# Kernel optimization log

Hardware: AMD Instinct MI355X
Metric: run time of the kernel (lower is better)

## Reference

```python
import jax, jax.numpy as jnp
import numpy as np

B, S, D = 16, 1024, 512
H, DH = 8, 64  # heads, dim_head


def setup_inputs() -> dict:
    key = jax.random.key(0)
    ks = jax.random.split(key, 7)
    x = jax.random.normal(ks[0], (B, S, D), dtype=jnp.float32)
    # variable sequence lengths in [1, S]
    seq_lens = jnp.maximum(jax.random.randint(ks[1], (B,), 0, S + 1), 1).astype(jnp.int32)
    w_std = 0.02
    Wq = jax.random.normal(ks[2], (D, D), dtype=jnp.float32) * w_std
    Wk = jax.random.normal(ks[3], (D, D), dtype=jnp.float32) * w_std
    Wv = jax.random.normal(ks[4], (D, D), dtype=jnp.float32) * w_std
    Wo = jax.random.normal(ks[5], (D, D), dtype=jnp.float32) * w_std
    bo = jnp.zeros((D,), dtype=jnp.float32)
    return {"x": x, "seq_lens": seq_lens, "Wq": Wq, "Wk": Wk, "Wv": Wv, "Wo": Wo, "bo": bo}


def reference(x, seq_lens, Wq, Wk, Wv, Wo, bo):
    # x: [B, S, D] padded ragged batch; seq_lens: [B] valid token counts.
    # Equivalent to the per-batch SDPA loop over jagged sequences: attention
    # is computed only among the valid tokens of each sequence.
    scale = DH ** -0.5
    q = (x @ Wq).reshape(B, S, H, DH)
    k = (x @ Wk).reshape(B, S, H, DH)
    v = (x @ Wv).reshape(B, S, H, DH)
    scores = jnp.einsum('bqhd,bkhd->bhqk', q, k) * scale  # [B,H,S,S]
    valid = jnp.arange(S)[None, :] < seq_lens[:, None]     # [B,S] token mask
    neg_inf = jnp.finfo(scores.dtype).min
    scores = jnp.where(valid[:, None, None, :], scores, neg_inf)
    attn = jax.nn.softmax(scores, axis=-1)
    out = jnp.einsum('bhqk,bkhd->bqhd', attn, v).reshape(B, S, D)
    out = out @ Wo + bo  # to_out Linear (dropout=0 / eval)
    return out * valid[:, :, None]  # zero padded query positions
```

## Files before the change

kernel.cpp:

```cpp
#include <hip/hip_runtime.h>
#include <hip/hip_bf16.h>

typedef __bf16 bf16_t;
typedef __attribute__((ext_vector_type(4))) __bf16 bf16x4;
typedef __attribute__((ext_vector_type(8))) __bf16 bf16x8;
typedef __attribute__((ext_vector_type(4))) float f32x4;

#define MFMA16(a, b, c) __builtin_amdgcn_mfma_f32_16x16x32_bf16((a), (b), (c), 0, 0, 0)

#define BB 16
#define SS 1024
#define DD 512
#define HH 8
#define DH 64
#define NTOK (BB * SS)
#define QSCALE 0.18033688f

typedef const __attribute__((address_space(1))) void gas_void;
typedef __attribute__((address_space(3))) void las_void;

__device__ __forceinline__ void async_cp16(const void* g, void* l) {
    __builtin_amdgcn_global_load_lds((gas_void*)g, (las_void*)l, 16, 0, 0);
}

__device__ __forceinline__ bf16x8 frag_ld(const char* sm, int row, int kk, int g) {
    int r7 = row & 7;
    int base = row * 128 + ((g & 1) << 3);
    int c0 = ((kk << 2) + (g >> 1)) ^ r7;
    int c1 = ((kk << 2) + 2 + (g >> 1)) ^ r7;
    bf16x4 lo = *(const bf16x4*)(sm + base + (c0 << 4));
    bf16x4 hi = *(const bf16x4*)(sm + base + (c1 << 4));
    return __builtin_shufflevector(lo, hi, 0, 1, 2, 3, 4, 5, 6, 7);
}

__device__ __forceinline__ bf16x8 fragl(const char* sm, int idx, int l) {
    return *(const bf16x8*)(sm + (idx * 64 + l) * 16);
}

__global__ __launch_bounds__(256) void transpose_w_k(const float* __restrict__ W0,
                                                     const float* __restrict__ W1,
                                                     const float* __restrict__ W2,
                                                     const float* __restrict__ W3,
                                                     bf16_t* __restrict__ Wt) {
    __shared__ float t[32][33];
    int z = blockIdx.z;
    const float* W = (z == 0) ? W0 : (z == 1) ? W1 : (z == 2) ? W2 : W3;
    bf16_t* out = Wt + (size_t)z * DD * DD;
    int n0 = blockIdx.x * 32, k0 = blockIdx.y * 32;
    int tx = threadIdx.x, ty = threadIdx.y;
#pragma unroll
    for (int i = 0; i < 32; i += 8)
        t[ty + i][tx] = W[(size_t)(k0 + ty + i) * DD + n0 + tx];
    __syncthreads();
#pragma unroll
    for (int i = 0; i < 32; i += 8)
        out[(size_t)(n0 + ty + i) * DD + k0 + tx] = (bf16_t)t[tx][ty + i];
}

__global__ void build_q_k(const int* __restrict__ sl, ushort* __restrict__ items,
                          int* __restrict__ meta) {
    int l = threadIdx.x;
    __shared__ int s_b[BB], s_cnt[BB], s_start[BB];
    if (l < BB) {
        int len = sl[l];
        int rank = 0;
        for (int j = 0; j < BB; ++j) {
            int lj = sl[j];
            if (lj > len || (lj == len && j < l)) ++rank;
        }
        s_b[rank] = l;
        s_cnt[rank] = (len + 63) >> 6;
    }
    __syncthreads();
    if (l < BB) {
        int st = 0;
        for (int j = 0; j < l; ++j) st += s_cnt[j];
        s_start[l] = st;
        if (l == BB - 1) meta[0] = st + s_cnt[l];
    }
    if (l >= 48 && l < 56) meta[1 + (l - 48)] = 0;
    __syncthreads();
    if (l < BB) {
        int b = s_b[l], st = s_start[l], c = s_cnt[l];
        for (int i = 0; i < c; ++i)
            items[st + i] = (ushort)((b << 4) | i);
    }
}

template <int MODE>
__global__ __launch_bounds__(256) void gemm_k(const float* __restrict__ Af,
                                              const bf16_t* __restrict__ A,
                                              const bf16_t* __restrict__ WtBase,
                                              bf16_t* __restrict__ oQ,
                                              bf16_t* __restrict__ oK,
                                              bf16_t* __restrict__ oVt,
                                              float* __restrict__ oO,
                                              const float* __restrict__ bo,
                                              const int* __restrict__ seq_lens) {
    __shared__ __align__(16) char smem[32768];
    char* smA = smem;
    char* smB = smem + 16384;
    const int tid = threadIdx.x;
    const int l = tid & 63, w = tid >> 6;
    const int lr = l & 15, g = l >> 4;
    const int bm = blockIdx.x, bn = blockIdx.y;
    const int z = (MODE == 0) ? blockIdx.z : 3;
    const bf16_t* Wt = WtBase + (size_t)z * DD * DD;
    const int row0 = bm * 128;
    const int col0 = bn * 128;
    const int wm = (w >> 1) * 64, wn = (w & 1) * 64;

    const int bb = row0 >> 10, s0 = row0 & 1023;
    const int len = seq_lens[bb];

    if (MODE == 0) {
        if (s0 >= ((len + 63) & ~63)) return;
    } else {
        if (s0 >= len) {
#pragma unroll
            for (int i = 0; i < 4; ++i) {
                int mrow = row0 + wm + i * 16 + g * 4;
#pragma unroll
                for (int j = 0; j < 4; ++j) {
                    int n = col0 + wn + j * 16 + lr;
#pragma unroll
                    for (int r = 0; r < 4; ++r)
                        oO[(size_t)(mrow + r) * DD + n] = 0.f;
                }
            }
            return;
        }
    }

    f32x4 acc[4][4] = {};

    for (int kt = 0; kt < 8; ++kt) {
        const int k0 = kt * 64;
        __syncthreads();
        if (MODE == 0) {
#pragma unroll
            for (int it = 0; it < 4; ++it) {
                int cl = it * 256 + tid;
                int m = cl >> 3, c = cl & 7;
                const float* src = Af + (size_t)(row0 + m) * DD + k0 + c * 8;
                float4 f0 = *(const float4*)(src);
                float4 f1 = *(const float4*)(src + 4);
                bf16x8 v;
                v[0] = (bf16_t)f0.x; v[1] = (bf16_t)f0.y;
                v[2] = (bf16_t)f0.z; v[3] = (bf16_t)f0.w;
                v[4] = (bf16_t)f1.x; v[5] = (bf16_t)f1.y;
                v[6] = (bf16_t)f1.z; v[7] = (bf16_t)f1.w;
                int cs = c ^ (m & 7);
                *(bf16x8*)(smA + (m * 8 + cs) * 16) = v;
            }
        } else {
#pragma unroll
            for (int it = 0; it < 4; ++it) {
                int cl = it * 256 + tid;
                int m = cl >> 3, p = cl & 7, c = p ^ (m & 7);
                async_cp16(A + (size_t)(row0 + m) * DD + k0 + c * 8, smA + cl * 16);
            }
        }
#pragma unroll
        for (int it = 0; it < 4; ++it) {
            int cl = it * 256 + tid;
            int m = cl >> 3, p = cl & 7, c = p ^ (m & 7);
            async_cp16(Wt + (size_t)(col0 + m) * DD + k0 + c * 8, smB + cl * 16);
        }
        __syncthreads();
#pragma unroll
        for (int kk = 0; kk < 2; ++kk) {
            bf16x8 af[4], bfr[4];
#pragma unroll
            for (int i = 0; i < 4; ++i) af[i] = frag_ld(smA, wm + i * 16 + lr, kk, g);
#pragma unroll
            for (int j = 0; j < 4; ++j) bfr[j] = frag_ld(smB, wn + j * 16 + lr, kk, g);
#pragma unroll
            for (int i = 0; i < 4; ++i)
#pragma unroll
                for (int j = 0; j < 4; ++j)
                    acc[i][j] = MFMA16(af[i], bfr[j], acc[i][j]);
        }
    }

    if (MODE == 0) {
        __syncthreads();
        char* tl = smem;
        const float sc = (z == 0) ? QSCALE : 1.f;
#pragma unroll
        for (int i = 0; i < 4; ++i)
#pragma unroll
            for (int j = 0; j < 4; ++j)
#pragma unroll
                for (int r = 0; r < 4; ++r) {
                    int s = wm + i * 16 + g * 4 + r;
                    int n = wn + j * 16 + lr;
                    int nb = 2 * n;
                    int byte = s * 256 + ((((nb >> 4) ^ (s & 7)) << 4) | (nb & 15));
                    *(bf16_t*)(tl + byte) = (bf16_t)(acc[i][j][r] * sc);
                }
        __syncthreads();
        const int b = bb;
        if (z < 2) {
            bf16_t* dst = (z == 0) ? oQ : oK;
#pragma unroll
            for (int c8 = 0; c8 < 8; ++c8) {
                int combo = c8 * 4 + w;
                int kk = combo & 1, t = (combo >> 1) & 7, hl = combo >> 4;
                int s = 16 * t + lr;
                bf16x4 pr[2];
#pragma unroll
                for (int jj = 0; jj < 2; ++jj) {
                    int nb = 128 * hl + 64 * kk + 32 * jj + 8 * g;
                    int byte = s * 256 + ((((nb >> 4) ^ (s & 7)) << 4) | (nb & 15));
                    pr[jj] = *(const bf16x4*)(tl + byte);
                }
                bf16x8 v = __builtin_shufflevector(pr[0], pr[1], 0, 1, 2, 3, 4, 5, 6, 7);
                int bhh = b * 8 + (col0 >> 6) + hl;
                int tg = (s0 >> 4) + t;
                *(bf16x8*)(dst + (((size_t)bhh * 64 + tg) * 2 + kk) * 512 + l * 8) = v;
            }
        } else {
#pragma unroll
            for (int c8 = 0; c8 < 8; ++c8) {
                int combo = c8 * 4 + w;
                int kk = combo & 1, dt = (combo >> 1) & 3;
                int st = (combo >> 3) & 1, hl = (combo >> 4) & 1;
                bf16x8 v;
#pragma unroll
                for (int j = 0; j < 8; ++j) {
                    int s = 64 * st + 32 * kk + 16 * (j >> 2) + 4 * g + (j & 3);
                    int n = 64 * hl + 16 * dt + lr;
                    int nb = 2 * n;
                    int byte = s * 256 + ((((nb >> 4) ^ (s & 7)) << 4) | (nb & 15));
                    v[j] = *(const bf16_t*)(tl + byte);
                }
                int bhh = b * 8 + (col0 >> 6) + hl;
                int stg = (s0 >> 6) + st;
                *(bf16x8*)(oVt + ((((size_t)bhh * 16 + stg) * 4 + dt) * 2 + kk) * 512 +
                           l * 8) = v;
            }
        }
    } else {
        const bool fullv = (s0 + 128 <= len);
#pragma unroll
        for (int i = 0; i < 4; ++i) {
            int mrow = row0 + wm + i * 16 + g * 4;
#pragma unroll
            for (int j = 0; j < 4; ++j) {
                int n = col0 + wn + j * 16 + lr;
                float bias = bo[n];
                if (fullv) {
#pragma unroll
                    for (int r = 0; r < 4; ++r)
                        oO[(size_t)(mrow + r) * DD + n] = acc[i][j][r] + bias;
                } else {
#pragma unroll
                    for (int r = 0; r < 4; ++r) {
                        int m = mrow + r;
                        int s = m & 1023;
                        oO[(size_t)m * DD + n] = (s < len) ? (acc[i][j][r] + bias) : 0.f;
                    }
                }
            }
        }
    }
}

__global__ __launch_bounds__(256) void attn_k(const bf16_t* __restrict__ Qf,
                                              const bf16_t* __restrict__ Kf,
                                              const bf16_t* __restrict__ Vf,
                                              bf16_t* __restrict__ O,
                                              const int* __restrict__ seq_lens,
                                              const ushort* __restrict__ items,
                                              int* __restrict__ meta) {
    __shared__ __align__(16) char smem[32768];
    __shared__ int s_item;
    const int tid = threadIdx.x, l = tid & 63, w = tid >> 6;
    const int lr = l & 15, g = l >> 4;
    const int nitems = meta[0];
    const int h = blockIdx.x & 7;
    int* cursor = meta + 1 + h;

    for (;;) {
        if (tid == 0) s_item = atomicAdd(cursor, 1);
        __syncthreads();
        const int ii = s_item;
        if (ii >= nitems) return;
        const int itv = items[ii];
        const int qt = itv & 15, b = itv >> 4;
        const int bh = b * 8 + h;
        const int len = seq_lens[b];
        const int q0 = qt * 64 + w * 16;

        const bf16_t* kfb = Kf + (size_t)bh * 65536;
        const bf16_t* vfb = Vf + (size_t)bh * 65536;

        bf16x8 bq[2];
        {
            size_t tb = ((size_t)bh * 64 + (q0 >> 4)) * 2;
            bq[0] = *(const bf16x8*)(Qf + (tb + 0) * 512 + l * 8);
            bq[1] = *(const bf16x8*)(Qf + (tb + 1) * 512 + l * 8);
        }

        f32x4 oacc[4] = {};
        float mrun = -1e30f, lpart = 0.f;

        const int nkt = (len + 63) >> 6;

        auto stage = [&](int buf, int kti) {
            char* smK = smem + buf * 16384;
            char* smV = smK + 8192;
            const bf16_t* ks = kfb + kti * 4096;
            const bf16_t* vs = vfb + kti * 4096;
            async_cp16(ks + tid * 8, smK + tid * 16);
            async_cp16(ks + (256 + tid) * 8, smK + (256 + tid) * 16);
            async_cp16(vs + tid * 8, smV + tid * 16);
            async_cp16(vs + (256 + tid) * 8, smV + (256 + tid) * 16);
        };

        stage(0, 0);
        int cur = 0;

        for (int kt = 0; kt < nkt; ++kt) {
            const int key0 = kt * 64;
            asm volatile("s_waitcnt vmcnt(0)" ::: "memory");
            __builtin_amdgcn_s_barrier();
            if (kt + 1 < nkt) stage(cur ^ 1, kt + 1);
            const char* smK = smem + cur * 16384;
            const char* smV = smK + 8192;

            f32x4 pacc[4] = {};
#pragma unroll
            for (int nt = 0; nt < 4; ++nt) {
                bf16x8 ak0 = fragl(smK, nt * 2 + 0, l);
                bf16x8 ak1 = fragl(smK, nt * 2 + 1, l);
                pacc[nt] = MFMA16(ak0, bq[0], pacc[nt]);
                pacc[nt] = MFMA16(ak1, bq[1], pacc[nt]);
            }

            const bool full = (key0 + 64 <= len);

            float mloc = -1e30f;
            if (full) {
#pragma unroll
                for (int nt = 0; nt < 4; ++nt)
#pragma unroll
                    for (int r = 0; r < 4; ++r) mloc = fmaxf(mloc, pacc[nt][r]);
            } else {
#pragma unroll
                for (int nt = 0; nt < 4; ++nt)
#pragma unroll
                    for (int r = 0; r < 4; ++r) {
                        int kg = key0 + nt * 16 + 4 * g + r;
                        float s = (kg < len) ? pacc[nt][r] : -1e30f;
                        pacc[nt][r] = s;
                        mloc = fmaxf(mloc, s);
                    }
            }
            mloc = fmaxf(mloc, __shfl_xor(mloc, 16, 64));
            mloc = fmaxf(mloc, __shfl_xor(mloc, 32, 64));

            if (!__all(mloc <= mrun + 8.f)) {
                float mn = fmaxf(mrun, mloc);
                float corr = __builtin_amdgcn_exp2f(mrun - mn);
                mrun = mn;
                lpart *= corr;
                float cb[4];
#pragma unroll
                for (int r = 0; r < 4; ++r) cb[r] = __shfl(corr, 4 * g + r, 64);
#pragma unroll
                for (int dt = 0; dt < 4; ++dt)
#pragma unroll
                    for (int r = 0; r < 4; ++r) oacc[dt][r] *= cb[r];
            }

            float ls = 0.f;
#pragma unroll
            for (int nt = 0; nt < 4; ++nt)
#pragma unroll
                for (int r = 0; r < 4; ++r) {
                    float p = __builtin_amdgcn_exp2f(pacc[nt][r] - mrun);
                    pacc[nt][r] = p;
                    ls += p;
                }
            lpart += ls;

            bf16x8 pa[2];
#pragma unroll
            for (int kf = 0; kf < 2; ++kf)
#pragma unroll
                for (int j = 0; j < 8; ++j)
                    pa[kf][j] = (bf16_t)pacc[2 * kf + (j >> 2)][j & 3];
#pragma unroll
            for (int kf = 0; kf < 2; ++kf)
#pragma unroll
                for (int dt = 0; dt < 4; ++dt) {
                    bf16x8 bv = fragl(smV, dt * 2 + kf, l);
                    oacc[dt] = MFMA16(pa[kf], bv, oacc[dt]);
                }
            cur ^= 1;
        }

        {
            float lt = lpart;
            lt += __shfl_xor(lt, 16, 64);
            lt += __shfl_xor(lt, 32, 64);
#pragma unroll
            for (int r = 0; r < 4; ++r) {
                float inv = 1.f / __shfl(lt, 4 * g + r, 64);
                int q = q0 + 4 * g + r;
                size_t orow = ((size_t)b * SS + q) * DD;
#pragma unroll
                for (int dt = 0; dt < 4; ++dt)
                    O[orow + h * DH + dt * 16 + lr] = (bf16_t)(oacc[dt][r] * inv);
            }
        }
    }
}

extern "C" void kernel_launch(void* const* d_in, const int* in_sizes, int n_in,
                              void* d_out, int out_size, void* d_ws, size_t ws_size,
                              hipStream_t stream) {
    const float* x = (const float*)d_in[0];
    const int* seq_lens = (const int*)d_in[1];
    const float* Wq = (const float*)d_in[2];
    const float* Wk = (const float*)d_in[3];
    const float* Wv = (const float*)d_in[4];
    const float* Wo = (const float*)d_in[5];
    const float* bo = (const float*)d_in[6];
    float* out = (float*)d_out;

    char* ws = (char*)d_ws;
    const size_t SEG = (size_t)NTOK * DD * sizeof(bf16_t);
    bf16_t* ab = (bf16_t*)ws;
    bf16_t* qb = (bf16_t*)(ws + SEG);
    bf16_t* kb = (bf16_t*)(ws + 2 * SEG);
    bf16_t* vtb = (bf16_t*)(ws + 3 * SEG);
    bf16_t* wt = (bf16_t*)(ws + 4 * SEG);
    ushort* items = (ushort*)(ws + 4 * SEG + (size_t)4 * DD * DD * sizeof(bf16_t));
    int* meta = (int*)(items + 4096);

    build_q_k<<<dim3(1), dim3(64), 0, stream>>>(seq_lens, items, meta);
    transpose_w_k<<<dim3(16, 16, 4), dim3(32, 8), 0, stream>>>(Wq, Wk, Wv, Wo, wt);
    gemm_k<0><<<dim3(NTOK / 128, DD / 128, 3), dim3(256), 0, stream>>>(
        x, nullptr, wt, qb, kb, vtb, nullptr, nullptr, seq_lens);
    attn_k<<<dim3(1280), dim3(256), 0, stream>>>(qb, kb, vtb, ab, seq_lens, items, meta);
    gemm_k<2><<<dim3(NTOK / 128, DD / 128, 1), dim3(256), 0, stream>>>(
        nullptr, ab, wt, nullptr, nullptr, nullptr, out, bo, seq_lens);
}
```

Baseline: 128.9 us.

## Double-buffer QKV projection GEMM with register prefetch of fp32 activations

New measurement: 133.0 us. +3.2%, slower.

```diff
diff --git a/kernel.cpp b/kernel.cpp
--- a/kernel.cpp
+++ b/kernel.cpp
@@ -97,9 +97,7 @@
                                               float* __restrict__ oO,
                                               const float* __restrict__ bo,
                                               const int* __restrict__ seq_lens) {
-    __shared__ __align__(16) char smem[32768];
-    char* smA = smem;
-    char* smB = smem + 16384;
+    __shared__ __align__(16) char smem[MODE == 0 ? 65536 : 32768];
     const int tid = threadIdx.x;
     const int l = tid & 63, w = tid >> 6;
     const int lr = l & 15, g = l >> 4;
@@ -134,52 +132,107 @@
 
     f32x4 acc[4][4] = {};
 
-    for (int kt = 0; kt < 8; ++kt) {
-        const int k0 = kt * 64;
-        __syncthreads();
-        if (MODE == 0) {
+    if (MODE == 0) {
+        float4 fa[4][2];
+        const int m_ = tid >> 3, c_ = tid & 7;
+        const int cs_ = c_ ^ (m_ & 7);
+
+        auto loadf = [&](int kt) {
+#pragma unroll
+            for (int it = 0; it < 4; ++it) {
+                const float* src =
+                    Af + (size_t)(row0 + it * 32 + m_) * DD + kt * 64 + c_ * 8;
+                fa[it][0] = *(const float4*)(src);
+                fa[it][1] = *(const float4*)(src + 4);
+            }
+        };
+        auto writeA = [&](char* sA) {
+#pragma unroll
+            for (int it = 0; it < 4; ++it) {
+                bf16x8 v;
+                v[0] = (bf16_t)fa[it][0].x; v[1] = (bf16_t)fa[it][0].y;
+                v[2] = (bf16_t)fa[it][0].z; v[3] = (bf16_t)fa[it][0].w;
+                v[4] = (bf16_t)fa[it][1].x; v[5] = (bf16_t)fa[it][1].y;
+                v[6] = (bf16_t)fa[it][1].z; v[7] = (bf16_t)fa[it][1].w;
+                *(bf16x8*)(sA + ((it * 32 + m_) * 8 + cs_) * 16) = v;
+            }
+        };
+        auto stageB = [&](char* sB, int kt) {
 #pragma unroll
             for (int it = 0; it < 4; ++it) {
                 int cl = it * 256 + tid;
-                int m = cl >> 3, c = cl & 7;
-                const float* src = Af + (size_t)(row0 + m) * DD + k0 + c * 8;
-                float4 f0 = *(const float4*)(src);
-                float4 f1 = *(const float4*)(src + 4);
-                bf16x8 v;
-                v[0] = (bf16_t)f0.x; v[1] = (bf16_t)f0.y;
-                v[2] = (bf16_t)f0.z; v[3] = (bf16_t)f0.w;
-                v[4] = (bf16_t)f1.x; v[5] = (bf16_t)f1.y;
-                v[6] = (bf16_t)f1.z; v[7] = (bf16_t)f1.w;
-                int cs = c ^ (m & 7);
-                *(bf16x8*)(smA + (m * 8 + cs) * 16) = v;
-            }
-        } else {
+                int m = cl >> 3, p = cl & 7, c = p ^ (m & 7);
+                async_cp16(Wt + (size_t)(col0 + m) * DD + kt * 64 + c * 8,
+                           sB + cl * 16);
+            }
+        };
+
+        loadf(0);
+        stageB(smem + 32768, 0);
+
+        for (int kt = 0; kt < 8; ++kt) {
+            char* sA = smem + (kt & 1) * 16384;
+            char* sB = smem + 32768 + (kt & 1) * 16384;
+            writeA(sA);
+            if (kt < 7) {
+                loadf(kt + 1);
+                stageB(smem + 32768 + ((kt + 1) & 1) * 16384, kt + 1);
+                asm volatile("s_waitcnt vmcnt(12) lgkmcnt(0)" ::: "memory");
+            } else {
+                asm volatile("s_waitcnt vmcnt(0) lgkmcnt(0)" ::: "memory");
+            }
+            __builtin_amdgcn_s_barrier();
+#pragma unroll
+            for (int kk = 0; kk < 2; ++kk) {
+                bf16x8 af[4], bfr[4];
+#pragma unroll
+                for (int i = 0; i < 4; ++i)
+                    af[i] = frag_ld(sA, wm + i * 16 + lr, kk, g);
+#pragma unroll
+                for (int j = 0; j < 4; ++j)
+                    bfr[j] = frag_ld(sB, wn + j * 16 + lr, kk, g);
+#pragma unroll
+                for (int i = 0; i < 4; ++i)
+#pragma unroll
+                    for (int j = 0; j < 4; ++j)
+                        acc[i][j] = MFMA16(af[i], bfr[j], acc[i][j]);
+            }
+            __builtin_amdgcn_s_barrier();
+        }
+    } else {
+        char* smA = smem;
+        char* smB = smem + 16384;
+        for (int kt = 0; kt < 8; ++kt) {
+            const int k0 = kt * 64;
+            __syncthreads();
 #pragma unroll
             for (int it = 0; it < 4; ++it) {
                 int cl = it * 256 + tid;
                 int m = cl >> 3, p = cl & 7, c = p ^ (m & 7);
                 async_cp16(A + (size_t)(row0 + m) * DD + k0 + c * 8, smA + cl * 16);
             }
-        }
-#pragma unroll
-        for (int it = 0; it < 4; ++it) {
-            int cl = it * 256 + tid;
-            int m = cl >> 3, p = cl & 7, c = p ^ (m & 7);
-            async_cp16(Wt + (size_t)(col0 + m) * DD + k0 + c * 8, smB + cl * 16);
-        }
-        __syncthreads();
-#pragma unroll
-        for (int kk = 0; kk < 2; ++kk) {
-            bf16x8 af[4], bfr[4];
-#pragma unroll
-            for (int i = 0; i < 4; ++i) af[i] = frag_ld(smA, wm + i * 16 + lr, kk, g);
-#pragma unroll
-            for (int j = 0; j < 4; ++j) bfr[j] = frag_ld(smB, wn + j * 16 + lr, kk, g);
-#pragma unroll
-            for (int i = 0; i < 4; ++i)
+#pragma unroll
+            for (int it = 0; it < 4; ++it) {
+                int cl = it * 256 + tid;
+                int m = cl >> 3, p = cl & 7, c = p ^ (m & 7);
+                async_cp16(Wt + (size_t)(col0 + m) * DD + k0 + c * 8, smB + cl * 16);
+            }
+            __syncthreads();
+#pragma unroll
+            for (int kk = 0; kk < 2; ++kk) {
+                bf16x8 af[4], bfr[4];
+#pragma unroll
+                for (int i = 0; i < 4; ++i)
+                    af[i] = frag_ld(smA, wm + i * 16 + lr, kk, g);
 #pragma unroll
                 for (int j = 0; j < 4; ++j)
-                    acc[i][j] = MFMA16(af[i], bfr[j], acc[i][j]);
+                    bfr[j] = frag_ld(smB, wn + j * 16 + lr, kk, g);
+#pragma unroll
+                for (int i = 0; i < 4; ++i)
+#pragma unroll
+                    for (int j = 0; j < 4; ++j)
+                        acc[i][j] = MFMA16(af[i], bfr[j], acc[i][j]);
+            }
         }
     }
 
```

## Fuse Q/K/V projections into one kernel sharing the converted x tile

Applied to the files above, without the earlier changes.

New measurement: 135.8 us. +5.3%, slower.

```diff
diff --git a/kernel.cpp b/kernel.cpp
--- a/kernel.cpp
+++ b/kernel.cpp
@@ -87,16 +87,146 @@
     }
 }
 
-template <int MODE>
-__global__ __launch_bounds__(256) void gemm_k(const float* __restrict__ Af,
-                                              const bf16_t* __restrict__ A,
-                                              const bf16_t* __restrict__ WtBase,
-                                              bf16_t* __restrict__ oQ,
-                                              bf16_t* __restrict__ oK,
-                                              bf16_t* __restrict__ oVt,
-                                              float* __restrict__ oO,
-                                              const float* __restrict__ bo,
-                                              const int* __restrict__ seq_lens) {
+__global__ __launch_bounds__(256) void qkv_k(const float* __restrict__ Af,
+                                             const bf16_t* __restrict__ WtBase,
+                                             bf16_t* __restrict__ oQ,
+                                             bf16_t* __restrict__ oK,
+                                             bf16_t* __restrict__ oVt,
+                                             const int* __restrict__ seq_lens) {
+    __shared__ __align__(16) char smem[65536];
+    const int tid = threadIdx.x;
+    const int l = tid & 63, w = tid >> 6;
+    const int lr = l & 15, g = l >> 4;
+    const int bm = blockIdx.x, bn = blockIdx.y;
+    const int row0 = bm * 128;
+    const int col0 = bn * 128;
+    const int wm = (w >> 1) * 64, wn = (w & 1) * 64;
+
+    const int b = row0 >> 10, s0 = row0 & 1023;
+    const int len = seq_lens[b];
+    if (s0 >= ((len + 63) & ~63)) return;
+
+    char* smA = smem;
+
+    f32x4 acc[3][4][4] = {};
+
+    const int m_ = tid >> 3, c_ = tid & 7;
+    const int cs_ = c_ ^ (m_ & 7);
+
+    for (int kt = 0; kt < 8; ++kt) {
+        const int k0 = kt * 64;
+        __syncthreads();
+#pragma unroll
+        for (int it = 0; it < 4; ++it) {
+            const float* src = Af + (size_t)(row0 + it * 32 + m_) * DD + k0 + c_ * 8;
+            float4 f0 = *(const float4*)(src);
+            float4 f1 = *(const float4*)(src + 4);
+            bf16x8 v;
+            v[0] = (bf16_t)f0.x; v[1] = (bf16_t)f0.y;
+            v[2] = (bf16_t)f0.z; v[3] = (bf16_t)f0.w;
+            v[4] = (bf16_t)f1.x; v[5] = (bf16_t)f1.y;
+            v[6] = (bf16_t)f1.z; v[7] = (bf16_t)f1.w;
+            *(bf16x8*)(smA + ((it * 32 + m_) * 8 + cs_) * 16) = v;
+        }
+#pragma unroll
+        for (int z = 0; z < 3; ++z) {
+            char* sB = smem + 16384 + z * 16384;
+            const bf16_t* Wt = WtBase + (size_t)z * DD * DD;
+#pragma unroll
+            for (int it = 0; it < 4; ++it) {
+                int cl = it * 256 + tid;
+                int m = cl >> 3, p = cl & 7, c = p ^ (m & 7);
+                async_cp16(Wt + (size_t)(col0 + m) * DD + k0 + c * 8, sB + cl * 16);
+            }
+        }
+        __syncthreads();
+#pragma unroll
+        for (int kk = 0; kk < 2; ++kk) {
+            bf16x8 af[4];
+#pragma unroll
+            for (int i = 0; i < 4; ++i) af[i] = frag_ld(smA, wm + i * 16 + lr, kk, g);
+#pragma unroll
+            for (int z = 0; z < 3; ++z) {
+                const char* sB = smem + 16384 + z * 16384;
+                bf16x8 bfr[4];
+#pragma unroll
+                for (int j = 0; j < 4; ++j)
+                    bfr[j] = frag_ld(sB, wn + j * 16 + lr, kk, g);
+#pragma unroll
+                for (int i = 0; i < 4; ++i)
+#pragma unroll
+                    for (int j = 0; j < 4; ++j)
+                        acc[z][i][j] = MFMA16(af[i], bfr[j], acc[z][i][j]);
+            }
+        }
+    }
+
+    char* tl = smem;
+#pragma unroll
+    for (int z = 0; z < 3; ++z) {
+        __syncthreads();
+        const float sc = (z == 0) ? QSCALE : 1.f;
+#pragma unroll
+        for (int i = 0; i < 4; ++i)
+#pragma unroll
+            for (int j = 0; j < 4; ++j)
+#pragma unroll
+                for (int r = 0; r < 4; ++r) {
+                    int s = wm + i * 16 + g * 4 + r;
+                    int n = wn + j * 16 + lr;
+                    int nb = 2 * n;
+                    int byte = s * 256 + ((((nb >> 4) ^ (s & 7)) << 4) | (nb & 15));
+                    *(bf16_t*)(tl + byte) = (bf16_t)(acc[z][i][j][r] * sc);
+                }
+        __syncthreads();
+        if (z < 2) {
+            bf16_t* dst = (z == 0) ? oQ : oK;
+#pragma unroll
+            for (int c8 = 0; c8 < 8; ++c8) {
+                int combo = c8 * 4 + w;
+                int kk = combo & 1, t = (combo >> 1) & 7, hl = combo >> 4;
+                int s = 16 * t + lr;
+                bf16x4 pr[2];
+#pragma unroll
+                for (int jj = 0; jj < 2; ++jj) {
+                    int nb = 128 * hl + 64 * kk + 32 * jj + 8 * g;
+                    int byte = s * 256 + ((((nb >> 4) ^ (s & 7)) << 4) | (nb & 15));
+                    pr[jj] = *(const bf16x4*)(tl + byte);
+                }
+                bf16x8 v = __builtin_shufflevector(pr[0], pr[1], 0, 1, 2, 3, 4, 5, 6, 7);
+                int bhh = b * 8 + (col0 >> 6) + hl;
+                int tg = (s0 >> 4) + t;
+                *(bf16x8*)(dst + (((size_t)bhh * 64 + tg) * 2 + kk) * 512 + l * 8) = v;
+            }
+        } else {
+#pragma unroll
+            for (int c8 = 0; c8 < 8; ++c8) {
+                int combo = c8 * 4 + w;
+                int kk = combo & 1, dt = (combo >> 1) & 3;
+                int st = (combo >> 3) & 1, hl = (combo >> 4) & 1;
+                bf16x8 v;
+#pragma unroll
+                for (int j = 0; j < 8; ++j) {
+                    int s = 64 * st + 32 * kk + 16 * (j >> 2) + 4 * g + (j & 3);
+                    int n = 64 * hl + 16 * dt + lr;
+                    int nb = 2 * n;
+                    int byte = s * 256 + ((((nb >> 4) ^ (s & 7)) << 4) | (nb & 15));
+                    v[j] = *(const bf16_t*)(tl + byte);
+                }
+                int bhh = b * 8 + (col0 >> 6) + hl;
+                int stg = (s0 >> 6) + st;
+                *(bf16x8*)(oVt + ((((size_t)bhh * 16 + stg) * 4 + dt) * 2 + kk) * 512 +
+                           l * 8) = v;
+            }
+        }
+    }
+}
+
+__global__ __launch_bounds__(256) void o_proj_k(const bf16_t* __restrict__ A,
+                                                const bf16_t* __restrict__ WtBase,
+                                                float* __restrict__ oO,
+                                                const float* __restrict__ bo,
+                                                const int* __restrict__ seq_lens) {
     __shared__ __align__(16) char smem[32768];
     char* smA = smem;
     char* smB = smem + 16384;
@@ -104,8 +234,7 @@
     const int l = tid & 63, w = tid >> 6;
     const int lr = l & 15, g = l >> 4;
     const int bm = blockIdx.x, bn = blockIdx.y;
-    const int z = (MODE == 0) ? blockIdx.z : 3;
-    const bf16_t* Wt = WtBase + (size_t)z * DD * DD;
+    const bf16_t* Wt = WtBase + (size_t)3 * DD * DD;
     const int row0 = bm * 128;
     const int col0 = bn * 128;
     const int wm = (w >> 1) * 64, wn = (w & 1) * 64;
@@ -113,23 +242,19 @@
     const int bb = row0 >> 10, s0 = row0 & 1023;
     const int len = seq_lens[bb];
 
-    if (MODE == 0) {
-        if (s0 >= ((len + 63) & ~63)) return;
-    } else {
-        if (s0 >= len) {
-#pragma unroll
-            for (int i = 0; i < 4; ++i) {
-                int mrow = row0 + wm + i * 16 + g * 4;
-#pragma unroll
-                for (int j = 0; j < 4; ++j) {
-                    int n = col0 + wn + j * 16 + lr;
-#pragma unroll
-                    for (int r = 0; r < 4; ++r)
-                        oO[(size_t)(mrow + r) * DD + n] = 0.f;
-                }
-            }
-            return;
-        }
+    if (s0 >= len) {
+#pragma unroll
+        for (int i = 0; i < 4; ++i) {
+            int mrow = row0 + wm + i * 16 + g * 4;
+#pragma unroll
+            for (int j = 0; j < 4; ++j) {
+                int n = col0 + wn + j * 16 + lr;
+#pragma unroll
+                for (int r = 0; r < 4; ++r)
+                    oO[(size_t)(mrow + r) * DD + n] = 0.f;
+            }
+        }
+        return;
     }
 
     f32x4 acc[4][4] = {};
@@ -137,29 +262,11 @@
     for (int kt = 0; kt < 8; ++kt) {
         const int k0 = kt * 64;
         __syncthreads();
-        if (MODE == 0) {
-#pragma unroll
-            for (int it = 0; it < 4; ++it) {
-                int cl = it * 256 + tid;
-                int m = cl >> 3, c = cl & 7;
-                const float* src = Af + (size_t)(row0 + m) * DD + k0 + c * 8;
-                float4 f0 = *(const float4*)(src);
-                float4 f1 = *(const float4*)(src + 4);
-                bf16x8 v;
-                v[0] = (bf16_t)f0.x; v[1] = (bf16_t)f0.y;
-                v[2] = (bf16_t)f0.z; v[3] = (bf16_t)f0.w;
-                v[4] = (bf16_t)f1.x; v[5] = (bf16_t)f1.y;
-                v[6] = (bf16_t)f1.z; v[7] = (bf16_t)f1.w;
-                int cs = c ^ (m & 7);
-                *(bf16x8*)(smA + (m * 8 + cs) * 16) = v;
-            }
-        } else {
-#pragma unroll
-            for (int it = 0; it < 4; ++it) {
-                int cl = it * 256 + tid;
-                int m = cl >> 3, p = cl & 7, c = p ^ (m & 7);
-                async_cp16(A + (size_t)(row0 + m) * DD + k0 + c * 8, smA + cl * 16);
-            }
+#pragma unroll
+        for (int it = 0; it < 4; ++it) {
+            int cl = it * 256 + tid;
+            int m = cl >> 3, p = cl & 7, c = p ^ (m & 7);
+            async_cp16(A + (size_t)(row0 + m) * DD + k0 + c * 8, smA + cl * 16);
         }
 #pragma unroll
         for (int it = 0; it < 4; ++it) {
@@ -183,84 +290,24 @@
         }
     }
 
-    if (MODE == 0) {
-        __syncthreads();
-        char* tl = smem;
-        const float sc = (z == 0) ? QSCALE : 1.f;
-#pragma unroll
-        for (int i = 0; i < 4; ++i)
-#pragma unroll
-            for (int j = 0; j < 4; ++j)
+    const bool fullv = (s0 + 128 <= len);
+#pragma unroll
+    for (int i = 0; i < 4; ++i) {
+        int mrow = row0 + wm + i * 16 + g * 4;
+#pragma unroll
+        for (int j = 0; j < 4; ++j) {
+            int n = col0 + wn + j * 16 + lr;
+            float bias = bo[n];
+            if (fullv) {
+#pragma unroll
+                for (int r = 0; r < 4; ++r)
+                    oO[(size_t)(mrow + r) * DD + n] = acc[i][j][r] + bias;
+            } else {
 #pragma unroll
                 for (int r = 0; r < 4; ++r) {
-                    int s = wm + i * 16 + g * 4 + r;
-                    int n = wn + j * 16 + lr;
-                    int nb = 2 * n;
-                    int byte = s * 256 + ((((nb >> 4) ^ (s & 7)) << 4) | (nb & 15));
-                    *(bf16_t*)(tl + byte) = (bf16_t)(acc[i][j][r] * sc);
-                }
-        __syncthreads();
-        const int b = bb;
-        if (z < 2) {
-            bf16_t* dst = (z == 0) ? oQ : oK;
-#pragma unroll
-            for (int c8 = 0; c8 < 8; ++c8) {
-                int combo = c8 * 4 + w;
-                int kk = combo & 1, t = (combo >> 1) & 7, hl = combo >> 4;
-                int s = 16 * t + lr;
-                bf16x4 pr[2];
-#pragma unroll
-                for (int jj = 0; jj < 2; ++jj) {
-                    int nb = 128 * hl + 64 * kk + 32 * jj + 8 * g;
-                    int byte = s * 256 + ((((nb >> 4) ^ (s & 7)) << 4) | (nb & 15));
-                    pr[jj] = *(const bf16x4*)(tl + byte);
-                }
-                bf16x8 v = __builtin_shufflevector(pr[0], pr[1], 0, 1, 2, 3, 4, 5, 6, 7);
-                int bhh = b * 8 + (col0 >> 6) + hl;
-                int tg = (s0 >> 4) + t;
-                *(bf16x8*)(dst + (((size_t)bhh * 64 + tg) * 2 + kk) * 512 + l * 8) = v;
-            }
-        } else {
-#pragma unroll
-            for (int c8 = 0; c8 < 8; ++c8) {
-                int combo = c8 * 4 + w;
-                int kk = combo & 1, dt = (combo >> 1) & 3;
-                int st = (combo >> 3) & 1, hl = (combo >> 4) & 1;
-                bf16x8 v;
-#pragma unroll
-                for (int j = 0; j < 8; ++j) {
-                    int s = 64 * st + 32 * kk + 16 * (j >> 2) + 4 * g + (j & 3);
-                    int n = 64 * hl + 16 * dt + lr;
-                    int nb = 2 * n;
-                    int byte = s * 256 + ((((nb >> 4) ^ (s & 7)) << 4) | (nb & 15));
-                    v[j] = *(const bf16_t*)(tl + byte);
-                }
-                int bhh = b * 8 + (col0 >> 6) + hl;
-                int stg = (s0 >> 6) + st;
-                *(bf16x8*)(oVt + ((((size_t)bhh * 16 + stg) * 4 + dt) * 2 + kk) * 512 +
-                           l * 8) = v;
-            }
-        }
-    } else {
-        const bool fullv = (s0 + 128 <= len);
-#pragma unroll
-        for (int i = 0; i < 4; ++i) {
-            int mrow = row0 + wm + i * 16 + g * 4;
-#pragma unroll
-            for (int j = 0; j < 4; ++j) {
-                int n = col0 + wn + j * 16 + lr;
-                float bias = bo[n];
-                if (fullv) {
-#pragma unroll
-                    for (int r = 0; r < 4; ++r)
-                        oO[(size_t)(mrow + r) * DD + n] = acc[i][j][r] + bias;
-                } else {
-#pragma unroll
-                    for (int r = 0; r < 4; ++r) {
-                        int m = mrow + r;
-                        int s = m & 1023;
-                        oO[(size_t)m * DD + n] = (s < len) ? (acc[i][j][r] + bias) : 0.f;
-                    }
+                    int m = mrow + r;
+                    int s = m & 1023;
+                    oO[(size_t)m * DD + n] = (s < len) ? (acc[i][j][r] + bias) : 0.f;
                 }
             }
         }
@@ -443,9 +490,9 @@
 
     build_q_k<<<dim3(1), dim3(64), 0, stream>>>(seq_lens, items, meta);
     transpose_w_k<<<dim3(16, 16, 4), dim3(32, 8), 0, stream>>>(Wq, Wk, Wv, Wo, wt);
-    gemm_k<0><<<dim3(NTOK / 128, DD / 128, 3), dim3(256), 0, stream>>>(
-        x, nullptr, wt, qb, kb, vtb, nullptr, nullptr, seq_lens);
+    qkv_k<<<dim3(NTOK / 128, DD / 128), dim3(256), 0, stream>>>(
+        x, wt, qb, kb, vtb, seq_lens);
     attn_k<<<dim3(1280), dim3(256), 0, stream>>>(qb, kb, vtb, ab, seq_lens, items, meta);
-    gemm_k<2><<<dim3(NTOK / 128, DD / 128, 1), dim3(256), 0, stream>>>(
-        nullptr, ab, wt, nullptr, nullptr, nullptr, out, bo, seq_lens);
-}
+    o_proj_k<<<dim3(NTOK / 128, DD / 128), dim3(256), 0, stream>>>(
+        ab, wt, out, bo, seq_lens);
+}
```
